# Kernel optimization log

Measured on AMD Instinct MI355X. Metric: run time of the kernel, lower is better.

The kernel has to match this reference:

```python
import jax, jax.numpy as jnp
import numpy as np

K = 100          # sliding window (even: matches torch pad (K//2, K//2-1) producing T windows)
EPS = 1e-12      # added to std, per original code


def setup_inputs() -> dict:
    key = jax.random.key(0)
    x = jax.random.normal(key, (8, 16384, 128), dtype=jnp.float32)  # B x T x D
    return {"x": x}


def _sliding_mean_std(x):
    """Per-frame sliding mean/std (unbiased, ddof=1) over a reflect-padded
    window of size K, via prefix sums: O(T) instead of O(T*K)."""
    B, T, D = x.shape
    # reflect pad the time axis: left K//2, right K//2-1 -> T + K - 1 frames
    xp = jnp.pad(x, ((0, 0), (K // 2, K // 2 - 1), (0, 0)), mode="reflect")
    zero = jnp.zeros((B, 1, D), dtype=x.dtype)
    cs = jnp.concatenate([zero, jnp.cumsum(xp, axis=1)], axis=1)        # (B, T+K, D)
    cs2 = jnp.concatenate([zero, jnp.cumsum(xp * xp, axis=1)], axis=1)  # (B, T+K, D)
    s = cs[:, K:K + T] - cs[:, 0:T]    # window sums,   (B, T, D)
    s2 = cs2[:, K:K + T] - cs2[:, 0:T]  # window sumsq, (B, T, D)
    m = s / K
    var = (s2 - K * m * m) / (K - 1)    # unbiased variance (torch.std default)
    std = jnp.sqrt(jnp.maximum(var, 0.0))
    return m, std


def reference(x) -> jnp.ndarray:
    # with_mean=True, with_std=True branch of MovingAvgNorm (T >= kernel_size)
    m, std = _sliding_mean_std(x)
    return (x - m) / (std + EPS)
```

## Files before the change

kernel.cpp:

```cpp
#include <hip/hip_runtime.h>

constexpr int KWIN = 100;
constexpr int HK   = 50;
constexpr int TSUB = 64;
constexpr int MB   = 8;
constexpr int PB   = 10;

template <bool REFLECT>
__device__ __forceinline__ int tidx(int t) {
    if constexpr (REFLECT) {
        constexpr int T = 16384;
        t = (t < 0) ? -t : t;
        return (t >= T) ? (2 * T - 2 - t) : t;
    } else {
        return t;
    }
}

template <bool REFLECT>
__device__ __forceinline__ void run_chunk(
    const float* __restrict__ xb, float* __restrict__ ob, const int t0)
{
    constexpr int D = 128;

    float v[KWIN];
    float sx = 0.f, sq = 0.f;

    #pragma unroll
    for (int jb = 0; jb < KWIN; jb += PB) {
        float g[PB];
        #pragma unroll
        for (int j = 0; j < PB; ++j)
            g[j] = xb[(size_t)tidx<REFLECT>(t0 - HK + jb + j) * D];
        #pragma unroll
        for (int j = 0; j < PB; ++j) {
            v[jb + j] = g[j];
            sx += g[j];
            sq  = fmaf(g[j], g[j], sq);
        }
    }

    const float invK   = 1.0f / (float)KWIN;
    const float invKm1 = 1.0f / (float)(KWIN - 1);
    const float fK     = (float)KWIN;

    #pragma unroll
    for (int tb = 0; tb < TSUB; tb += MB) {
        float g[MB];
        #pragma unroll
        for (int j = 0; j < MB; ++j)
            g[j] = xb[(size_t)tidx<REFLECT>(t0 + tb + j + HK) * D];
        #pragma unroll
        for (int j = 0; j < MB; ++j) {
            const int jj = tb + j;
            const float c = v[(jj + HK) % KWIN];
            const float o = v[jj % KWIN];
            const float m  = sx * invK;
            const float va = fmaxf((sq - fK * m * m) * invKm1, 1e-24f);
            const float rs = __builtin_amdgcn_rsqf(va);
            ob[(size_t)(t0 + jj) * D] = (c - m) * rs;
            sx += g[j] - o;
            sq += g[j] * g[j] - o * o;
            v[jj % KWIN] = g[j];
        }
    }
}

__global__ __launch_bounds__(256, 2) void man_kernel(
    const float* __restrict__ x, float* __restrict__ out)
{
    constexpr int T = 16384, D = 128;

    const int i     = blockIdx.x;
    const int bb    = (i & 7) * 128 + (i >> 3);
    const int b     = bb >> 7;
    const int cpair = bb & 127;
    const int w     = threadIdx.x >> 7;
    const int tid   = threadIdx.x & 127;
    const int t0    = (cpair * 2 + w) * TSUB;

    const float* __restrict__ xb = x   + (size_t)b * T * D + tid;
    float*       __restrict__ ob = out + (size_t)b * T * D + tid;

    if (t0 >= HK && t0 + TSUB - 1 + HK < T) {
        run_chunk<false>(xb, ob, t0);
    } else {
        run_chunk<true>(xb, ob, t0);
    }
}

extern "C" void kernel_launch(void* const* d_in, const int* in_sizes, int n_in,
                              void* d_out, int out_size, void* d_ws, size_t ws_size,
                              hipStream_t stream) {
    (void)in_sizes; (void)n_in; (void)d_ws; (void)ws_size; (void)out_size;
    const float* x = (const float*)d_in[0];
    float* out = (float*)d_out;
    man_kernel<<<dim3(1024), dim3(256), 0, stream>>>(x, out);
}
```

Baseline: 33.87 us.

## Shrink register ring to half window and re-load outgoing samples with double-buffered loads

Replaces the 100-entry register window with a 50-entry ring holding only the upcoming center samples. Samples leaving the window are re-read from global memory, which is likely cache-resident. Loads are double-buffered so each group of eight is fetched ahead of its compute, and outputs use nontemporal stores. This is meant to cut VGPR pressure and expose more memory-level parallelism, at the cost of extra global loads.

```diff
diff --git a/kernel.cpp b/kernel.cpp
--- a/kernel.cpp
+++ b/kernel.cpp
@@ -4,7 +4,7 @@
 constexpr int HK   = 50;
 constexpr int TSUB = 64;
 constexpr int MB   = 8;
-constexpr int PB   = 10;
+constexpr int PB   = 25;
 
 template <bool REFLECT>
 __device__ __forceinline__ int tidx(int t) {
@@ -12,58 +12,93 @@
         constexpr int T = 16384;
         t = (t < 0) ? -t : t;
         return (t >= T) ? (2 * T - 2 - t) : t;
-    } else {
-        return t;
     }
+    return t;
 }
 
 template <bool REFLECT>
 __device__ __forceinline__ void run_chunk(
     const float* __restrict__ xb, float* __restrict__ ob, const int t0)
 {
-    constexpr int D = 128;
-
-    float v[KWIN];
+    float ring[HK];
     float sx = 0.f, sq = 0.f;
 
-    #pragma unroll
-    for (int jb = 0; jb < KWIN; jb += PB) {
-        float g[PB];
+    {
+        float la[PB], lb[PB];
         #pragma unroll
         for (int j = 0; j < PB; ++j)
-            g[j] = xb[(size_t)tidx<REFLECT>(t0 - HK + jb + j) * D];
+            la[j] = xb[(size_t)tidx<REFLECT>(t0 - HK + j) * 128];
         #pragma unroll
-        for (int j = 0; j < PB; ++j) {
-            v[jb + j] = g[j];
-            sx += g[j];
-            sq  = fmaf(g[j], g[j], sq);
-        }
+        for (int j = 0; j < PB; ++j)
+            lb[j] = xb[(size_t)tidx<REFLECT>(t0 - PB + j) * 128];
+        #pragma unroll
+        for (int j = 0; j < PB; ++j) { sx += la[j]; sq = fmaf(la[j], la[j], sq); }
+        #pragma unroll
+        for (int j = 0; j < PB; ++j)
+            ring[j] = xb[(size_t)tidx<REFLECT>(t0 + j) * 128];
+        #pragma unroll
+        for (int j = 0; j < PB; ++j) { sx += lb[j]; sq = fmaf(lb[j], lb[j], sq); }
+        #pragma unroll
+        for (int j = 0; j < PB; ++j)
+            ring[PB + j] = xb[(size_t)tidx<REFLECT>(t0 + PB + j) * 128];
+        #pragma unroll
+        for (int j = 0; j < PB; ++j) { sx += ring[j]; sq = fmaf(ring[j], ring[j], sq); }
+        #pragma unroll
+        for (int j = 0; j < PB; ++j) { sx += ring[PB + j]; sq = fmaf(ring[PB + j], ring[PB + j], sq); }
     }
 
     const float invK   = 1.0f / (float)KWIN;
     const float invKm1 = 1.0f / (float)(KWIN - 1);
     const float fK     = (float)KWIN;
 
-    #pragma unroll
-    for (int tb = 0; tb < TSUB; tb += MB) {
-        float g[MB];
-        #pragma unroll
-        for (int j = 0; j < MB; ++j)
-            g[j] = xb[(size_t)tidx<REFLECT>(t0 + tb + j + HK) * D];
-        #pragma unroll
-        for (int j = 0; j < MB; ++j) {
-            const int jj = tb + j;
-            const float c = v[(jj + HK) % KWIN];
-            const float o = v[jj % KWIN];
-            const float m  = sx * invK;
-            const float va = fmaxf((sq - fK * m * m) * invKm1, 1e-24f);
-            const float rs = __builtin_amdgcn_rsqf(va);
-            ob[(size_t)(t0 + jj) * D] = (c - m) * rs;
-            sx += g[j] - o;
-            sq += g[j] * g[j] - o * o;
-            v[jj % KWIN] = g[j];
-        }
+    float inA[MB], outA[MB], inB[MB], outB[MB];
+
+#define LOADB(IN, OUT, KB)                                                    \
+    {                                                                         \
+        _Pragma("unroll")                                                     \
+        for (int j = 0; j < MB; ++j) {                                        \
+            const int t = t0 + (KB) + j;                                      \
+            IN[j]  = xb[(size_t)tidx<REFLECT>(t + HK) * 128];                 \
+            OUT[j] = xb[(size_t)tidx<REFLECT>(t - HK) * 128];                 \
+        }                                                                     \
     }
+
+#define COMPUTEB(IN, OUT, KB)                                                 \
+    {                                                                         \
+        _Pragma("unroll")                                                     \
+        for (int j = 0; j < MB; ++j) {                                        \
+            const int k = (KB) + j;                                           \
+            const float c  = ring[k % HK];                                    \
+            const float m  = sx * invK;                                       \
+            const float va = fmaxf((sq - fK * m * m) * invKm1, 1e-24f);       \
+            const float rs = __builtin_amdgcn_rsqf(va);                       \
+            __builtin_nontemporal_store((c - m) * rs,                         \
+                                        &ob[(size_t)(t0 + k) * 128]);         \
+            sx += IN[j] - OUT[j];                                             \
+            sq += IN[j] * IN[j] - OUT[j] * OUT[j];                            \
+            ring[k % HK] = IN[j];                                             \
+        }                                                                     \
+    }
+
+    LOADB(inA, outA, 0 * MB);
+    LOADB(inB, outB, 1 * MB);
+    COMPUTEB(inA, outA, 0 * MB);
+    LOADB(inA, outA, 2 * MB);
+    COMPUTEB(inB, outB, 1 * MB);
+    LOADB(inB, outB, 3 * MB);
+    COMPUTEB(inA, outA, 2 * MB);
+    LOADB(inA, outA, 4 * MB);
+    COMPUTEB(inB, outB, 3 * MB);
+    LOADB(inB, outB, 5 * MB);
+    COMPUTEB(inA, outA, 4 * MB);
+    LOADB(inA, outA, 6 * MB);
+    COMPUTEB(inB, outB, 5 * MB);
+    LOADB(inB, outB, 7 * MB);
+    COMPUTEB(inA, outA, 6 * MB);
+    COMPUTEB(inB, outB, 7 * MB);
+
+#undef LOADB
+#undef COMPUTEB
 }
 
 __global__ __launch_bounds__(256, 2) void man_kernel(
@@ -71,13 +106,13 @@
 {
     constexpr int T = 16384, D = 128;
 
-    const int i     = blockIdx.x;
-    const int bb    = (i & 7) * 128 + (i >> 3);
-    const int b     = bb >> 7;
-    const int cpair = bb & 127;
-    const int w     = threadIdx.x >> 7;
-    const int tid   = threadIdx.x & 127;
-    const int t0    = (cpair * 2 + w) * TSUB;
+    const int i   = blockIdx.x;
+    const int bb  = (i & 7) * 128 + (i >> 3);
+    const int b   = bb >> 7;
+    const int seg = bb & 127;
+    const int w   = threadIdx.x >> 7;
+    const int tid = threadIdx.x & 127;
+    const int t0  = (seg * 2 + w) * TSUB;
 
     const float* __restrict__ xb = x   + (size_t)b * T * D + tid;
     float*       __restrict__ ob = out + (size_t)b * T * D + tid;
```

New measurement: 30.00 us. -11.4%, faster.
